# Optimization experiments

Measured on AMD Instinct MI355X. Metric: run time of the kernel, lower is better.

Reference implementation:

```python
import jax, jax.numpy as jnp
import numpy as np

B, C, O, H, W, E, K = 16, 128, 128, 128, 128, 3, 3


def setup_inputs() -> dict:
    key = jax.random.key(0)
    k1, k2, k3, k4 = jax.random.split(key, 4)
    q = jax.random.normal(k1, (B, C, H, W), dtype=jnp.float32)
    y = jax.random.normal(k2, (B, C, H, W), dtype=jnp.float32)
    experts = jax.random.normal(k3, (E, O, 2 * C, K, K), dtype=jnp.float32)
    gate_w = jax.random.normal(k4, (2 * C, E), dtype=jnp.float32) * 0.02
    gate_b = jnp.zeros((E,), dtype=jnp.float32)
    return {"q": q, "y": y, "experts": experts, "gate_w": gate_w, "gate_b": gate_b}


def reference(q, y, experts, gate_w, gate_b):
    # gating: global-average-pool y, duplicate channels, linear + softmax over experts
    y_ctx = y.mean(axis=(2, 3))                       # [B, C]
    context = jnp.concatenate([y_ctx, y_ctx], axis=1)  # [B, 2C]
    gates = jax.nn.softmax(context @ gate_w + gate_b, axis=1)  # [B, E]

    # per-sample aggregated conv kernel (weighted sum over experts)
    agg = jnp.einsum('be,eoikl->boikl', gates, experts)  # [B, O, 2C, K, K]

    xy = jnp.concatenate([q, q], axis=1)  # [B, 2C, H, W]

    # per-sample conv2d with its own kernel, stride 1, padding k//2 == SAME for odd K
    def conv1(x, w):
        # x: [2C, H, W], w: [O, 2C, K, K]
        return jax.lax.conv_general_dilated(x[None], w, window_strides=(1, 1), padding='SAME')[0]

    out = jax.vmap(conv1)(xy, agg)  # [B, O, H, W]
    return out
```

## Files before the change

kernel.cpp:

```cpp
#include <hip/hip_runtime.h>
#include <hip/hip_bf16.h>

typedef unsigned short ushort_t;
typedef __attribute__((ext_vector_type(8)))  short bf16x8;
typedef __attribute__((ext_vector_type(16))) float f32x16;

#define NB 16
#define NC 128
#define NO 128
#define NH 128
#define NW 128
#define NE 3

__device__ __forceinline__ ushort_t f2bf(float f) {
    __hip_bfloat16 h = __float2bfloat16(f);
    return *reinterpret_cast<ushort_t*>(&h);
}

__device__ __forceinline__ void gld_lds16(const void* g, void* l) {
    __builtin_amdgcn_global_load_lds(
        (const __attribute__((address_space(1))) unsigned int*)g,
        (__attribute__((address_space(3))) unsigned int*)l,
        16, 0, 0);
}

__global__ void mean_kernel(const float* __restrict__ y, float* __restrict__ yctx) {
    const int bc = blockIdx.x;
    const float4* p = (const float4*)(y + (size_t)bc * 16384);
    float s = 0.f;
    for (int i = threadIdx.x; i < 4096; i += 256) {
        float4 v = p[i];
        s += (v.x + v.y) + (v.z + v.w);
    }
#pragma unroll
    for (int off = 32; off > 0; off >>= 1) s += __shfl_down(s, off);
    __shared__ float red[4];
    const int wv = threadIdx.x >> 6, lane = threadIdx.x & 63;
    if (lane == 0) red[wv] = s;
    __syncthreads();
    if (threadIdx.x == 0)
        yctx[bc] = (red[0] + red[1] + red[2] + red[3]) * (1.f / 16384.f);
}

__global__ void gate_kernel(const float* __restrict__ yctx, const float* __restrict__ gw,
                            const float* __restrict__ gb, float* __restrict__ gates) {
    __shared__ float lg[NB][NE];
    const int t = threadIdx.x;
    if (t < NB * NE) {
        const int b = t / NE, e = t % NE;
        float s = gb[e];
        const float* yc = yctx + b * NC;
        for (int c = 0; c < NC; ++c)
            s += yc[c] * (gw[c * NE + e] + gw[(c + NC) * NE + e]);
        lg[b][e] = s;
    }
    __syncthreads();
    if (t < NB) {
        float a0 = lg[t][0], a1 = lg[t][1], a2 = lg[t][2];
        float m = fmaxf(a0, fmaxf(a1, a2));
        float e0 = expf(a0 - m), e1 = expf(a1 - m), e2 = expf(a2 - m);
        float inv = 1.f / (e0 + e1 + e2);
        gates[t * 3 + 0] = e0 * inv;
        gates[t * 3 + 1] = e1 * inv;
        gates[t * 3 + 2] = e2 * inv;
    }
}

__global__ void qtrans_kernel(const float* __restrict__ q, ushort_t* __restrict__ qT) {
    const int h = blockIdx.x, b = blockIdx.y;
    const int t = threadIdx.x;
    const int wseg = (t & 31) * 4;
#pragma unroll
    for (int ii = 0; ii < 2; ++ii) {
        const int cg = (t >> 5) + 8 * ii;
        float vt[8][4];
#pragma unroll
        for (int k = 0; k < 8; ++k) {
            float4 v = *(const float4*)(q + ((size_t)(b * NC + cg * 8 + k) * 16384 + h * NW + wseg));
            vt[k][0] = v.x; vt[k][1] = v.y; vt[k][2] = v.z; vt[k][3] = v.w;
        }
#pragma unroll
        for (int i = 0; i < 4; ++i) {
            unsigned int u[8];
#pragma unroll
            for (int k = 0; k < 8; ++k) u[k] = f2bf(vt[k][i]);
            uint4 pk;
            pk.x = u[0] | (u[1] << 16);
            pk.y = u[2] | (u[3] << 16);
            pk.z = u[4] | (u[5] << 16);
            pk.w = u[6] | (u[7] << 16);
            *(uint4*)&qT[(size_t)(b * NH + h) * 16384 + (size_t)(cg * 128 + wseg + i) * 8] = pk;
        }
    }
}

__global__ void wfold_kernel(const float* __restrict__ experts, const float* __restrict__ gates,
                             ushort_t* __restrict__ wfrag) {
    const int blk = blockIdx.x;
    const int b = blk >> 5, cc = (blk >> 2) & 7, m = blk & 3;
    __shared__ __align__(16) ushort_t tile[9 * 64 * 8];
    const int t = threadIdx.x;
    float gg[3];
    gg[0] = gates[b * 3 + 0]; gg[1] = gates[b * 3 + 1]; gg[2] = gates[b * 3 + 2];
    const int obase = m * 32, cbase = cc * 16;
#pragma unroll
    for (int oi = 0; oi < 2; ++oi) {
        const int o = (t >> 4) + 16 * oi;
        const int c = (t & 15);
        float w9[9];
#pragma unroll
        for (int k = 0; k < 9; ++k) w9[k] = 0.f;
#pragma unroll
        for (int e = 0; e < 3; ++e) {
            const float ge = gg[e];
            const float* p1 = experts + ((size_t)((e * NO) + obase + o) * 256 + cbase + c) * 9;
            const float* p2 = p1 + 128 * 9;
#pragma unroll
            for (int k = 0; k < 9; ++k) w9[k] += ge * (p1[k] + p2[k]);
        }
        const int lf = ((c >> 3) << 5) | o;
#pragma unroll
        for (int k = 0; k < 9; ++k) tile[(k * 64 + lf) * 8 + (c & 7)] = f2bf(w9[k]);
    }
    __syncthreads();
    ushort_t* dst = wfrag + (size_t)((b * 8 + cc) * 4 + m) * 4608;
    for (int u = t; u < 576; u += 256)
        ((uint4*)dst)[u] = ((const uint4*)tile)[u];
}

__global__ __launch_bounds__(256, 2)
void conv_kernel(const ushort_t* __restrict__ qT, const ushort_t* __restrict__ wfrag,
                 float* __restrict__ out) {
    const int b  = blockIdx.y;
    const int h0 = blockIdx.x * 2;
    const int tid  = threadIdx.x;
    const int wv   = tid >> 6;
    const int lane = tid & 63;
    const int l31  = lane & 31;
    const int g    = lane >> 5;

    __shared__ __align__(16) ushort_t A_lds[4 * 9 * 64 * 8];
    __shared__ __align__(16) ushort_t q_lds[4 * 2 * 130 * 8];

    if (tid < 16) {
        const int qr = tid >> 2, hg = (tid >> 1) & 1, cl = (tid & 1) * 129;
        uint4 zz; zz.x = zz.y = zz.z = zz.w = 0u;
        *(uint4*)&q_lds[((qr * 2 + hg) * 130 + cl) * 8] = zz;
    }

    f32x16 acc[4][2];
#pragma unroll
    for (int mi = 0; mi < 4; ++mi)
#pragma unroll
        for (int ni = 0; ni < 2; ++ni)
#pragma unroll
            for (int r = 0; r < 16; ++r) acc[mi][ni][r] = 0.f;

    const int qrow_s = wv;
    const int hprime = h0 + qrow_s - 1;
    const bool hvalid = (hprime >= 0) && (hprime < NH);

    for (int cc = 0; cc < 8; ++cc) {
        {
            const ushort_t* wb = wfrag + (size_t)(((b * 8 + cc) * 4 + wv)) * 4608;
#pragma unroll
            for (int t = 0; t < 9; ++t)
                gld_lds16(wb + (t * 64 + lane) * 8, &A_lds[((wv * 9 + t) * 64) * 8]);
        }
        if (hvalid) {
            const ushort_t* qb = qT + (size_t)((b * NH + hprime) * 16 + cc * 2) * 1024;
#pragma unroll
            for (int hg = 0; hg < 2; ++hg)
#pragma unroll
                for (int it = 0; it < 2; ++it)
                    gld_lds16(qb + hg * 1024 + (it * 64 + lane) * 8,
                              &q_lds[((qrow_s * 2 + hg) * 130 + 1 + it * 64) * 8]);
        } else {
            uint4 zz; zz.x = zz.y = zz.z = zz.w = 0u;
#pragma unroll
            for (int hg = 0; hg < 2; ++hg)
#pragma unroll
                for (int it = 0; it < 2; ++it)
                    *(uint4*)&q_lds[((qrow_s * 2 + hg) * 130 + 1 + it * 64 + lane) * 8] = zz;
        }
        __syncthreads();

#pragma unroll
        for (int kh = 0; kh < 3; ++kh) {
#pragma unroll
            for (int kw = 0; kw < 3; ++kw) {
                const int t = kh * 3 + kw;
                bf16x8 afr[4];
#pragma unroll
                for (int mi = 0; mi < 4; ++mi)
                    afr[mi] = *(const bf16x8*)&A_lds[((mi * 9 + t) * 64 + lane) * 8];
                bf16x8 bfr[2];
#pragma unroll
                for (int ni = 0; ni < 2; ++ni) {
                    const int n  = wv * 2 + ni;
                    const int r  = n >> 2;
                    const int w0 = (n & 3) * 32;
                    const int qrow = r + kh;
                    const int col  = w0 + l31 + kw;
                    bfr[ni] = *(const bf16x8*)&q_lds[((qrow * 2 + g) * 130 + col) * 8];
                }
#pragma unroll
                for (int mi = 0; mi < 4; ++mi)
#pragma unroll
                    for (int ni = 0; ni < 2; ++ni)
                        acc[mi][ni] = __builtin_amdgcn_mfma_f32_32x32x16_bf16(
                            afr[mi], bfr[ni], acc[mi][ni], 0, 0, 0);
            }
        }
        __syncthreads();
    }

#pragma unroll
    for (int mi = 0; mi < 4; ++mi) {
#pragma unroll
        for (int ni = 0; ni < 2; ++ni) {
            const int n  = wv * 2 + ni;
            const int r  = n >> 2;
            const int w0 = (n & 3) * 32;
            const int hh = h0 + r;
            float* ob = out + ((size_t)(b * NO + mi * 32) * NH + hh) * NW + w0 + l31;
#pragma unroll
            for (int reg = 0; reg < 16; ++reg) {
                const int row = (reg & 3) + 8 * (reg >> 2) + 4 * g;
                ob[(size_t)row * (NH * NW)] = acc[mi][ni][reg];
            }
        }
    }
}

extern "C" void kernel_launch(void* const* d_in, const int* in_sizes, int n_in,
                              void* d_out, int out_size, void* d_ws, size_t ws_size,
                              hipStream_t stream) {
    (void)in_sizes; (void)n_in; (void)out_size; (void)ws_size;
    const float* q       = (const float*)d_in[0];
    const float* y       = (const float*)d_in[1];
    const float* experts = (const float*)d_in[2];
    const float* gate_w  = (const float*)d_in[3];
    const float* gate_b  = (const float*)d_in[4];
    float* out = (float*)d_out;

    char* ws = (char*)d_ws;
    float*    yctx  = (float*)ws;
    float*    gates = (float*)(ws + 8192);
    ushort_t* wfrag = (ushort_t*)(ws + 16384);
    ushort_t* qT    = (ushort_t*)(ws + 4734976);

    mean_kernel<<<2048, 256, 0, stream>>>(y, yctx);
    gate_kernel<<<1, 64, 0, stream>>>(yctx, gate_w, gate_b, gates);
    qtrans_kernel<<<dim3(NH, NB), 256, 0, stream>>>(q, qT);
    wfold_kernel<<<512, 256, 0, stream>>>(experts, gates, wfrag);
    conv_kernel<<<dim3(NH / 2, NB), 256, 0, stream>>>(qT, wfrag, out);
}
```

Baseline: 401.6 us.

## Split conv output channels across blocks, remap grid for XCD locality, rework qtrans

The conv kernel now splits the 128 output channels into two halves per block, which doubles the grid to 2048 blocks. Each wave computes one 32-channel M tile by four 32-wide N tiles, and the launch bound rises to 4 blocks per CU. Block IDs are remapped so that the 8 blocks sharing an XCD cover neighbouring row pairs, improving L2 reuse of q rows. The q transpose kernel is rewritten so that each thread packs 8 channels for one column using strided scalar loads. The trade-off is that each q tile is now loaded twice, once per channel half, and the per-wave reuse of B fragments drops.

```diff
diff --git a/kernel.cpp b/kernel.cpp
--- a/kernel.cpp
+++ b/kernel.cpp
@@ -69,28 +69,22 @@
 __global__ void qtrans_kernel(const float* __restrict__ q, ushort_t* __restrict__ qT) {
     const int h = blockIdx.x, b = blockIdx.y;
     const int t = threadIdx.x;
-    const int wseg = (t & 31) * 4;
-#pragma unroll
-    for (int ii = 0; ii < 2; ++ii) {
-        const int cg = (t >> 5) + 8 * ii;
-        float vt[8][4];
-#pragma unroll
-        for (int k = 0; k < 8; ++k) {
-            float4 v = *(const float4*)(q + ((size_t)(b * NC + cg * 8 + k) * 16384 + h * NW + wseg));
-            vt[k][0] = v.x; vt[k][1] = v.y; vt[k][2] = v.z; vt[k][3] = v.w;
-        }
-#pragma unroll
-        for (int i = 0; i < 4; ++i) {
-            unsigned int u[8];
-#pragma unroll
-            for (int k = 0; k < 8; ++k) u[k] = f2bf(vt[k][i]);
-            uint4 pk;
-            pk.x = u[0] | (u[1] << 16);
-            pk.y = u[2] | (u[3] << 16);
-            pk.z = u[4] | (u[5] << 16);
-            pk.w = u[6] | (u[7] << 16);
-            *(uint4*)&qT[(size_t)(b * NH + h) * 16384 + (size_t)(cg * 128 + wseg + i) * 8] = pk;
-        }
+    const float* qb = q + (size_t)b * NC * 16384 + h * NW;
+    ushort_t* dst = qT + (size_t)(b * NH + h) * 16384;
+#pragma unroll
+    for (int kk = 0; kk < 8; ++kk) {
+        const int u = t + 256 * kk;
+        const int cg = u >> 7, w = u & 127;
+        const float* p = qb + (size_t)(cg * 8) * 16384 + w;
+        unsigned int uu[8];
+#pragma unroll
+        for (int j = 0; j < 8; ++j) uu[j] = f2bf(p[(size_t)j * 16384]);
+        uint4 pk;
+        pk.x = uu[0] | (uu[1] << 16);
+        pk.y = uu[2] | (uu[3] << 16);
+        pk.z = uu[4] | (uu[5] << 16);
+        pk.w = uu[6] | (uu[7] << 16);
+        *(uint4*)&dst[(size_t)u * 8] = pk;
     }
 }
 
@@ -128,18 +122,24 @@
         ((uint4*)dst)[u] = ((const uint4*)tile)[u];
 }
 
-__global__ __launch_bounds__(256, 2)
+__global__ __launch_bounds__(256, 4)
 void conv_kernel(const ushort_t* __restrict__ qT, const ushort_t* __restrict__ wfrag,
                  float* __restrict__ out) {
-    const int b  = blockIdx.y;
-    const int h0 = blockIdx.x * 2;
+    const int lid = blockIdx.x;
+    const int xcd = lid & 7;
+    const int r   = lid >> 3;
+    const int b   = r >> 4;
+    const int s   = r & 15;
+    const int mhalf = s & 1;
+    const int h0  = (xcd * 8 + (s >> 1)) * 2;
+
     const int tid  = threadIdx.x;
     const int wv   = tid >> 6;
     const int lane = tid & 63;
     const int l31  = lane & 31;
     const int g    = lane >> 5;
 
-    __shared__ __align__(16) ushort_t A_lds[4 * 9 * 64 * 8];
+    __shared__ __align__(16) ushort_t A_lds[2 * 9 * 64 * 8];
     __shared__ __align__(16) ushort_t q_lds[4 * 2 * 130 * 8];
 
     if (tid < 16) {
@@ -148,40 +148,40 @@
         *(uint4*)&q_lds[((qr * 2 + hg) * 130 + cl) * 8] = zz;
     }
 
-    f32x16 acc[4][2];
-#pragma unroll
-    for (int mi = 0; mi < 4; ++mi)
-#pragma unroll
-        for (int ni = 0; ni < 2; ++ni)
-#pragma unroll
-            for (int r = 0; r < 16; ++r) acc[mi][ni][r] = 0.f;
-
-    const int qrow_s = wv;
-    const int hprime = h0 + qrow_s - 1;
-    const bool hvalid = (hprime >= 0) && (hprime < NH);
+    f32x16 acc[4];
+#pragma unroll
+    for (int j = 0; j < 4; ++j)
+#pragma unroll
+        for (int rr = 0; rr < 16; ++rr) acc[j][rr] = 0.f;
+
+    const int myM = wv >> 1;
+    const int ng  = wv & 1;
+
+    const int hp = h0 + wv - 1;
+    const bool hvalid = (hp >= 0) && (hp < NH);
 
     for (int cc = 0; cc < 8; ++cc) {
-        {
-            const ushort_t* wb = wfrag + (size_t)(((b * 8 + cc) * 4 + wv)) * 4608;
+        if (wv < 2) {
+            const ushort_t* wb = wfrag + (size_t)((b * 8 + cc) * 4 + mhalf * 2 + wv) * 4608;
 #pragma unroll
             for (int t = 0; t < 9; ++t)
                 gld_lds16(wb + (t * 64 + lane) * 8, &A_lds[((wv * 9 + t) * 64) * 8]);
         }
         if (hvalid) {
-            const ushort_t* qb = qT + (size_t)((b * NH + hprime) * 16 + cc * 2) * 1024;
+            const ushort_t* qb = qT + (size_t)(b * NH + hp) * 16384 + cc * 2048;
 #pragma unroll
             for (int hg = 0; hg < 2; ++hg)
 #pragma unroll
                 for (int it = 0; it < 2; ++it)
                     gld_lds16(qb + hg * 1024 + (it * 64 + lane) * 8,
-                              &q_lds[((qrow_s * 2 + hg) * 130 + 1 + it * 64) * 8]);
+                              &q_lds[((wv * 2 + hg) * 130 + 1 + it * 64) * 8]);
         } else {
             uint4 zz; zz.x = zz.y = zz.z = zz.w = 0u;
 #pragma unroll
             for (int hg = 0; hg < 2; ++hg)
 #pragma unroll
                 for (int it = 0; it < 2; ++it)
-                    *(uint4*)&q_lds[((qrow_s * 2 + hg) * 130 + 1 + it * 64 + lane) * 8] = zz;
+                    *(uint4*)&q_lds[((wv * 2 + hg) * 130 + 1 + it * 64 + lane) * 8] = zz;
         }
         __syncthreads();
 
@@ -190,45 +190,27 @@
 #pragma unroll
             for (int kw = 0; kw < 3; ++kw) {
                 const int t = kh * 3 + kw;
-                bf16x8 afr[4];
-#pragma unroll
-                for (int mi = 0; mi < 4; ++mi)
-                    afr[mi] = *(const bf16x8*)&A_lds[((mi * 9 + t) * 64 + lane) * 8];
-                bf16x8 bfr[2];
-#pragma unroll
-                for (int ni = 0; ni < 2; ++ni) {
-                    const int n  = wv * 2 + ni;
-                    const int r  = n >> 2;
-                    const int w0 = (n & 3) * 32;
-                    const int qrow = r + kh;
-                    const int col  = w0 + l31 + kw;
-                    bfr[ni] = *(const bf16x8*)&q_lds[((qrow * 2 + g) * 130 + col) * 8];
+                bf16x8 afr = *(const bf16x8*)&A_lds[((myM * 9 + t) * 64 + lane) * 8];
+#pragma unroll
+                for (int j = 0; j < 4; ++j) {
+                    const int col = j * 32 + l31 + kw;
+                    bf16x8 bfr = *(const bf16x8*)&q_lds[(((ng + kh) * 2 + g) * 130 + col) * 8];
+                    acc[j] = __builtin_amdgcn_mfma_f32_32x32x16_bf16(afr, bfr, acc[j], 0, 0, 0);
                 }
-#pragma unroll
-                for (int mi = 0; mi < 4; ++mi)
-#pragma unroll
-                    for (int ni = 0; ni < 2; ++ni)
-                        acc[mi][ni] = __builtin_amdgcn_mfma_f32_32x32x16_bf16(
-                            afr[mi], bfr[ni], acc[mi][ni], 0, 0, 0);
             }
         }
         __syncthreads();
     }
 
-#pragma unroll
-    for (int mi = 0; mi < 4; ++mi) {
-#pragma unroll
-        for (int ni = 0; ni < 2; ++ni) {
-            const int n  = wv * 2 + ni;
-            const int r  = n >> 2;
-            const int w0 = (n & 3) * 32;
-            const int hh = h0 + r;
-            float* ob = out + ((size_t)(b * NO + mi * 32) * NH + hh) * NW + w0 + l31;
-#pragma unroll
-            for (int reg = 0; reg < 16; ++reg) {
-                const int row = (reg & 3) + 8 * (reg >> 2) + 4 * g;
-                ob[(size_t)row * (NH * NW)] = acc[mi][ni][reg];
-            }
+    const int obase = mhalf * 64 + myM * 32;
+    const int hh = h0 + ng;
+#pragma unroll
+    for (int j = 0; j < 4; ++j) {
+        float* ob = out + ((size_t)(b * NO + obase) * NH + hh) * NW + j * 32 + l31;
+#pragma unroll
+        for (int reg = 0; reg < 16; ++reg) {
+            const int row = (reg & 3) + 8 * (reg >> 2) + 4 * g;
+            ob[(size_t)row * (NH * NW)] = acc[j][reg];
         }
     }
 }
@@ -254,5 +236,5 @@
     gate_kernel<<<1, 64, 0, stream>>>(yctx, gate_w, gate_b, gates);
     qtrans_kernel<<<dim3(NH, NB), 256, 0, stream>>>(q, qT);
     wfold_kernel<<<512, 256, 0, stream>>>(experts, gates, wfrag);
-    conv_kernel<<<dim3(NH / 2, NB), 256, 0, stream>>>(qT, wfrag, out);
-}
+    conv_kernel<<<2048, 256, 0, stream>>>(qT, wfrag, out);
+}
```

Result: no change. 396.6 us (-1.2%).
